# Optimization experiments

Hardware: AMD Instinct MI355X
Metric: run time of the kernel (lower is better)

The kernel has to match this reference:

```python
import jax, jax.numpy as jnp
import numpy as np
import math

B, T, C, H = 4, 4096, 1024, 16
D = C // H

def setup_inputs() -> dict:
    key = jax.random.key(0)
    k1, k2, k3, k4, k5 = jax.random.split(key, 5)
    s = 1.0 / math.sqrt(C)
    return {
        "x": jax.random.normal(k1, (B, T, C), dtype=jnp.float32),
        "W_qkv": jax.random.normal(k2, (C, 3 * C), dtype=jnp.float32) * s,
        "b_qkv": jax.random.normal(k3, (3 * C,), dtype=jnp.float32) * 0.01,
        "W_out": jax.random.normal(k4, (C, C), dtype=jnp.float32) * s,
        "b_out": jax.random.normal(k5, (C,), dtype=jnp.float32) * 0.01,
    }

def reference(x, W_qkv, b_qkv, W_out, b_out):
    qkv = x @ W_qkv + b_qkv                      # (B,T,3C)
    q, k, v = jnp.split(qkv, 3, axis=2)
    q = q.reshape(B, T, H, D)
    k = k.reshape(B, T, H, D)
    v = v.reshape(B, T, H, D)
    # attention over the HEAD axis per (B,T): scores (B,T,H,H)
    att = jnp.einsum('bthd,btgd->bthg', q, k) / math.sqrt(D)
    att = jax.nn.softmax(att, axis=-1)
    out = jnp.einsum('bthg,btgd->bthd', att, v)  # (B,T,H,D)
    out = out.reshape(B, T, C)
    return out @ W_out + b_out
```

## Files before the change

### kernel.cpp

```cpp
#include <hip/hip_runtime.h>
#include <cstdint>
#include <cstddef>

constexpr int Bc = 4;
constexpr int Tc = 4096;
constexpr int Cc = 1024;
constexpr int Hc = 16;
constexpr int Dc = 64;
constexpr int Mc = Bc * Tc;
constexpr int N1c = 3 * Cc;
constexpr int Kc = Cc;
constexpr int KBc = Kc / 32;

typedef __bf16 bf16x8 __attribute__((ext_vector_type(8)));
typedef float  f32x4  __attribute__((ext_vector_type(4)));

__device__ __forceinline__ float bf2f(unsigned short u) {
    return __uint_as_float(((unsigned)u) << 16);
}
__device__ __forceinline__ unsigned short f2bf(float f) {
    unsigned u = __float_as_uint(f);
    u += 0x7FFF + ((u >> 16) & 1);
    return (unsigned short)(u >> 16);
}


__global__ void convert_x_packed(const float* __restrict__ x,
                                 unsigned short* __restrict__ Ap) {
    const int w = threadIdx.x >> 6, lane = threadIdx.x & 63;
    const int t = blockIdx.x * 4 + w;
    const int mb = t >> 5, kb = t & 31;
    const int r = lane >> 2, c = lane & 3;
    const float* src = x + (size_t)(mb * 16 + r) * Kc + kb * 32 + c * 8;
    float4 f0 = *(const float4*)src;
    float4 f1 = *(const float4*)(src + 4);
    unsigned short u[8];
    u[0] = f2bf(f0.x); u[1] = f2bf(f0.y); u[2] = f2bf(f0.z); u[3] = f2bf(f0.w);
    u[4] = f2bf(f1.x); u[5] = f2bf(f1.y); u[6] = f2bf(f1.z); u[7] = f2bf(f1.w);
    *(uint4*)(Ap + (size_t)t * 512 + (c * 16 + r) * 8) = *(uint4*)u;
}

__global__ void transpose_convert_packed(const float* __restrict__ W,
                                         unsigned short* __restrict__ Bp,
                                         int K, int N) {
    __shared__ float tile[32][33];
    const int tx = threadIdx.x, ty = threadIdx.y;
    const int n0 = blockIdx.x * 32, k0 = blockIdx.y * 32;
    for (int i = ty; i < 32; i += 8)
        tile[i][tx] = W[(size_t)(k0 + i) * N + n0 + tx];
    __syncthreads();
    const int t = ty * 32 + tx;
    const int h = t >> 7, rr = t & 127, lane = rr >> 1, half = rr & 1;
    const int fq = lane >> 4, fn = lane & 15;
    unsigned short u[4];
    #pragma unroll
    for (int j = 0; j < 4; ++j)
        u[j] = f2bf(tile[fq * 8 + half * 4 + j][h * 16 + fn]);
    size_t tileIdx = (size_t)((n0 >> 4) + h) * (K >> 5) + (k0 >> 5);
    *(uint2*)(Bp + tileIdx * 512 + lane * 8 + half * 4) = *(uint2*)u;
}

template <bool OUT_BF16>
__global__ __launch_bounds__(256, 3) void flat_gemm_kernel(
    const unsigned short* __restrict__ Ap,
    const unsigned short* __restrict__ Bp,
    const float* __restrict__ bias,
    void* __restrict__ Cout,
    int M, int N, int K) {
    const int KB = K >> 5;
    const int w    = threadIdx.x >> 6;
    const int lane = threadIdx.x & 63;
    const int m0 = blockIdx.y * 128;
    const int n0 = blockIdx.x * 128;
    const int wm = (w >> 1) * 64;
    const int wn = (w & 1) * 64;

    const unsigned short* Abase = Ap + (size_t)(((m0 + wm) >> 4) * KB) * 512 + lane * 8;
    const unsigned short* Bbase = Bp + (size_t)(((n0 + wn) >> 4) * KB) * 512 + lane * 8;
    const int miStride = KB * 512;
    const int kbStride = 512;

    const f32x4 zero4 = {0.f, 0.f, 0.f, 0.f};
    f32x4 acc[4][4];
    #pragma unroll
    for (int i = 0; i < 4; ++i)
        #pragma unroll
        for (int j = 0; j < 4; ++j) acc[i][j] = zero4;

    bf16x8 a0[4], b0[4], a1[4], b1[4];
    #pragma unroll
    for (int mi = 0; mi < 4; ++mi) a0[mi] = *(const bf16x8*)(Abase + mi * miStride);
    #pragma unroll
    for (int ni = 0; ni < 4; ++ni) b0[ni] = *(const bf16x8*)(Bbase + ni * miStride);

    #pragma unroll 1
    for (int kb = 0; kb < KB; kb += 2) {
        #pragma unroll
        for (int mi = 0; mi < 4; ++mi)
            a1[mi] = *(const bf16x8*)(Abase + mi * miStride + (kb + 1) * kbStride);
        #pragma unroll
        for (int ni = 0; ni < 4; ++ni)
            b1[ni] = *(const bf16x8*)(Bbase + ni * miStride + (kb + 1) * kbStride);
        #pragma unroll
        for (int mi = 0; mi < 4; ++mi)
            #pragma unroll
            for (int ni = 0; ni < 4; ++ni)
                acc[mi][ni] = __builtin_amdgcn_mfma_f32_16x16x32_bf16(
                    a0[mi], b0[ni], acc[mi][ni], 0, 0, 0);
        if (kb + 2 < KB) {
            #pragma unroll
            for (int mi = 0; mi < 4; ++mi)
                a0[mi] = *(const bf16x8*)(Abase + mi * miStride + (kb + 2) * kbStride);
            #pragma unroll
            for (int ni = 0; ni < 4; ++ni)
                b0[ni] = *(const bf16x8*)(Bbase + ni * miStride + (kb + 2) * kbStride);
        }
        #pragma unroll
        for (int mi = 0; mi < 4; ++mi)
            #pragma unroll
            for (int ni = 0; ni < 4; ++ni)
                acc[mi][ni] = __builtin_amdgcn_mfma_f32_16x16x32_bf16(
                    a1[mi], b1[ni], acc[mi][ni], 0, 0, 0);
    }

    const int fr = lane & 15;
    const int fq = lane >> 4;
    #pragma unroll
    for (int mi = 0; mi < 4; ++mi) {
        #pragma unroll
        for (int ni = 0; ni < 4; ++ni) {
            int row = m0 + wm + mi * 16 + fq * 4;
            int col = n0 + wn + ni * 16 + fr;
            float bb = bias[col];
            #pragma unroll
            for (int r = 0; r < 4; ++r) {
                float v = acc[mi][ni][r] + bb;
                if (OUT_BF16)
                    ((unsigned short*)Cout)[(size_t)(row + r) * N + col] = f2bf(v);
                else
                    ((float*)Cout)[(size_t)(row + r) * N + col] = v;
            }
        }
    }
}

__global__ __launch_bounds__(256) void attn_mfma_kernel(
    const unsigned short* __restrict__ qkv,
    unsigned short* __restrict__ attP) {
    __shared__ char smem[4 * 3584];
    const int w    = threadIdx.x >> 6;
    const int lane = threadIdx.x & 63;
    const int m    = lane & 15;
    const int q    = lane >> 4;
    const int row  = blockIdx.x * 4 + w;
    unsigned short* sV = (unsigned short*)(smem + w * 3584);
    float*          sP = (float*)(smem + w * 3584 + 2304);

    const unsigned short* src = qkv + (size_t)row * 3072;

    bf16x8 aq0 = *(const bf16x8*)(src + m * 64 + q * 8);
    bf16x8 aq1 = *(const bf16x8*)(src + m * 64 + 32 + q * 8);
    bf16x8 bk0 = *(const bf16x8*)(src + 1024 + m * 64 + q * 8);
    bf16x8 bk1 = *(const bf16x8*)(src + 1024 + m * 64 + 32 + q * 8);

    #pragma unroll
    for (int t = 0; t < 2; ++t) {
        int G = t * 64 + lane;
        int r = G >> 3, p = G & 7;
        *(uint4*)(sV + r * 72 + p * 8) = *(const uint4*)(src + 2048 + G * 8);
    }

    f32x4 s = {0.f, 0.f, 0.f, 0.f};
    s = __builtin_amdgcn_mfma_f32_16x16x32_bf16(aq0, bk0, s, 0, 0, 0);
    s = __builtin_amdgcn_mfma_f32_16x16x32_bf16(aq1, bk1, s, 0, 0, 0);

    #pragma unroll
    for (int r = 0; r < 4; ++r) {
        float t0 = s[r] * 0.125f;
        float mx = t0;
        mx = fmaxf(mx, __shfl_xor(mx, 1));
        mx = fmaxf(mx, __shfl_xor(mx, 2));
        mx = fmaxf(mx, __shfl_xor(mx, 4));
        mx = fmaxf(mx, __shfl_xor(mx, 8));
        float e = __expf(t0 - mx);
        float su = e;
        su += __shfl_xor(su, 1);
        su += __shfl_xor(su, 2);
        su += __shfl_xor(su, 4);
        su += __shfl_xor(su, 8);
        sP[(q * 4 + r) * 20 + m] = e / su;
    }
    __syncthreads();

    const float* pr = sP + m * 20 + (q & 1) * 8;
    float4 pf0 = *(const float4*)(pr);
    float4 pf1 = *(const float4*)(pr + 4);
    const bool act = (q < 2);
    union { unsigned short u[8]; bf16x8 b; } pa;
    pa.u[0] = act ? f2bf(pf0.x) : 0;
    pa.u[1] = act ? f2bf(pf0.y) : 0;
    pa.u[2] = act ? f2bf(pf0.z) : 0;
    pa.u[3] = act ? f2bf(pf0.w) : 0;
    pa.u[4] = act ? f2bf(pf1.x) : 0;
    pa.u[5] = act ? f2bf(pf1.y) : 0;
    pa.u[6] = act ? f2bf(pf1.z) : 0;
    pa.u[7] = act ? f2bf(pf1.w) : 0;

    const unsigned short* vb = sV + (q & 1) * 8 * 72;
    const size_t tileBase = (size_t)(row >> 4) * 32 * 512;
    const int fr_tok = row & 15;
    #pragma unroll
    for (int c4 = 0; c4 < 4; ++c4) {
        union { unsigned short u[8]; bf16x8 b; } vf;
        #pragma unroll
        for (int j = 0; j < 8; ++j) vf.u[j] = vb[j * 72 + c4 * 16 + m];
        f32x4 o = {0.f, 0.f, 0.f, 0.f};
        o = __builtin_amdgcn_mfma_f32_16x16x32_bf16(pa.b, vf.b, o, 0, 0, 0);
        #pragma unroll
        for (int r = 0; r < 4; ++r) {
            int col = (q * 4 + r) * 64 + c4 * 16 + m;
            size_t off = tileBase + (size_t)(col >> 5) * 512
                       + (((col >> 3) & 3) * 16 + fr_tok) * 8 + (col & 7);
            attP[off] = f2bf(o[r]);
        }
    }
}

extern "C" void kernel_launch(void* const* d_in, const int* in_sizes, int n_in,
                              void* d_out, int out_size, void* d_ws, size_t ws_size,
                              hipStream_t stream) {
    const float* x    = (const float*)d_in[0];
    const float* Wqkv = (const float*)d_in[1];
    const float* bqkv = (const float*)d_in[2];
    const float* Wout = (const float*)d_in[3];
    const float* bout = (const float*)d_in[4];
    float* out = (float*)d_out;

    char* ws = (char*)d_ws;
    unsigned short* xp   = (unsigned short*)ws;                 ws += (size_t)Mc * Kc * 2;
    unsigned short* Wqkp = (unsigned short*)ws;                 ws += (size_t)N1c * Kc * 2;
    unsigned short* Wop  = (unsigned short*)ws;                 ws += (size_t)Cc * Kc * 2;
    unsigned short* qkv  = (unsigned short*)ws;
    unsigned short* attP = xp;

    convert_x_packed<<<(Mc / 16) * KBc / 4, 256, 0, stream>>>(x, xp);
    transpose_convert_packed<<<dim3(N1c / 32, Kc / 32), dim3(32, 8), 0, stream>>>(Wqkv, Wqkp, Kc, N1c);
    transpose_convert_packed<<<dim3(Cc / 32, Kc / 32), dim3(32, 8), 0, stream>>>(Wout, Wop, Kc, Cc);
    flat_gemm_kernel<true><<<dim3(N1c / 128, Mc / 128), 256, 0, stream>>>(xp, Wqkp, bqkv, qkv, Mc, N1c, Kc);
    attn_mfma_kernel<<<Mc / 4, 256, 0, stream>>>(qkv, attP);
    flat_gemm_kernel<false><<<dim3(Cc / 128, Mc / 128), 256, 0, stream>>>(attP, Wop, bout, out, Mc, Cc, Kc);
}
```

Before: 336.8 us.

## Add XCD-aware GEMM block swizzle, row-major attention output with separate repack

The GEMM grid becomes 1D and block ids are remapped so that each XCD handles a contiguous band of M tiles, grouped 8 at a time, to improve L2 reuse of the A and B tiles. The attention kernel now writes its output row-major, giving coalesced stores instead of scattered packed-tile stores. A new repack kernel then converts that output into the packed layout the GEMM expects. The GEMM occupancy hint is raised from 3 to 4 blocks per SM. The cost is an extra kernel launch and an extra 32MB round trip through memory, plus more register pressure in the GEMM.

```diff
diff --git a/kernel.cpp b/kernel.cpp
--- a/kernel.cpp
+++ b/kernel.cpp
@@ -40,6 +40,16 @@
     *(uint4*)(Ap + (size_t)t * 512 + (c * 16 + r) * 8) = *(uint4*)u;
 }
 
+__global__ void repack_bf16_packed(const unsigned short* __restrict__ src,
+                                   unsigned short* __restrict__ Ap) {
+    const int w = threadIdx.x >> 6, lane = threadIdx.x & 63;
+    const int t = blockIdx.x * 4 + w;
+    const int mb = t >> 5, kb = t & 31;
+    const int r = lane >> 2, c = lane & 3;
+    uint4 v = *(const uint4*)(src + (size_t)(mb * 16 + r) * Kc + kb * 32 + c * 8);
+    *(uint4*)(Ap + (size_t)t * 512 + (c * 16 + r) * 8) = v;
+}
+
 __global__ void transpose_convert_packed(const float* __restrict__ W,
                                          unsigned short* __restrict__ Bp,
                                          int K, int N) {
@@ -61,17 +71,27 @@
 }
 
 template <bool OUT_BF16>
-__global__ __launch_bounds__(256, 3) void flat_gemm_kernel(
+__global__ __launch_bounds__(256, 4) void flat_gemm_kernel(
     const unsigned short* __restrict__ Ap,
     const unsigned short* __restrict__ Bp,
     const float* __restrict__ bias,
     void* __restrict__ Cout,
-    int M, int N, int K) {
+    int M, int N, int K, int NB) {
     const int KB = K >> 5;
+    const int MB = M >> 7;
+    const int id   = blockIdx.x;
+    const int xcd  = id & 7;
+    const int per  = id >> 3;
+    const int MSTR = MB >> 3;
+    const int byl  = per & 7;
+    const int bx   = (per >> 3) % NB;
+    const int pass = per / (8 * NB);
+    const int by   = xcd * MSTR + pass * 8 + byl;
+
     const int w    = threadIdx.x >> 6;
     const int lane = threadIdx.x & 63;
-    const int m0 = blockIdx.y * 128;
-    const int n0 = blockIdx.x * 128;
+    const int m0 = by * 128;
+    const int n0 = bx * 128;
     const int wm = (w >> 1) * 64;
     const int wn = (w & 1) * 64;
 
@@ -146,7 +166,7 @@
 
 __global__ __launch_bounds__(256) void attn_mfma_kernel(
     const unsigned short* __restrict__ qkv,
-    unsigned short* __restrict__ attP) {
+    unsigned short* __restrict__ att) {
     __shared__ char smem[4 * 3584];
     const int w    = threadIdx.x >> 6;
     const int lane = threadIdx.x & 63;
@@ -207,8 +227,7 @@
     pa.u[7] = act ? f2bf(pf1.w) : 0;
 
     const unsigned short* vb = sV + (q & 1) * 8 * 72;
-    const size_t tileBase = (size_t)(row >> 4) * 32 * 512;
-    const int fr_tok = row & 15;
+    unsigned short* dst = att + (size_t)row * 1024;
     #pragma unroll
     for (int c4 = 0; c4 < 4; ++c4) {
         union { unsigned short u[8]; bf16x8 b; } vf;
@@ -216,13 +235,12 @@
         for (int j = 0; j < 8; ++j) vf.u[j] = vb[j * 72 + c4 * 16 + m];
         f32x4 o = {0.f, 0.f, 0.f, 0.f};
         o = __builtin_amdgcn_mfma_f32_16x16x32_bf16(pa.b, vf.b, o, 0, 0, 0);
-        #pragma unroll
-        for (int r = 0; r < 4; ++r) {
-            int col = (q * 4 + r) * 64 + c4 * 16 + m;
-            size_t off = tileBase + (size_t)(col >> 5) * 512
-                       + (((col >> 3) & 3) * 16 + fr_tok) * 8 + (col & 7);
-            attP[off] = f2bf(o[r]);
-        }
+        unsigned short outv[4];
+        #pragma unroll
+        for (int r = 0; r < 4; ++r) outv[r] = f2bf(o[r]);
+        #pragma unroll
+        for (int r = 0; r < 4; ++r)
+            dst[(q * 4 + r) * 64 + c4 * 16 + m] = outv[r];
     }
 }
 
@@ -237,16 +255,20 @@
     float* out = (float*)d_out;
 
     char* ws = (char*)d_ws;
-    unsigned short* xp   = (unsigned short*)ws;                 ws += (size_t)Mc * Kc * 2;
-    unsigned short* Wqkp = (unsigned short*)ws;                 ws += (size_t)N1c * Kc * 2;
-    unsigned short* Wop  = (unsigned short*)ws;                 ws += (size_t)Cc * Kc * 2;
-    unsigned short* qkv  = (unsigned short*)ws;
-    unsigned short* attP = xp;
+    unsigned short* xp    = (unsigned short*)ws;                ws += (size_t)Mc * Kc * 2;
+    unsigned short* Wqkp  = (unsigned short*)ws;                ws += (size_t)N1c * Kc * 2;
+    unsigned short* Wop   = (unsigned short*)ws;                ws += (size_t)Cc * Kc * 2;
+    unsigned short* qkv   = (unsigned short*)ws;                ws += (size_t)Mc * N1c * 2;
+    unsigned short* attRM = (unsigned short*)ws;
+    unsigned short* attP  = xp;
 
     convert_x_packed<<<(Mc / 16) * KBc / 4, 256, 0, stream>>>(x, xp);
     transpose_convert_packed<<<dim3(N1c / 32, Kc / 32), dim3(32, 8), 0, stream>>>(Wqkv, Wqkp, Kc, N1c);
     transpose_convert_packed<<<dim3(Cc / 32, Kc / 32), dim3(32, 8), 0, stream>>>(Wout, Wop, Kc, Cc);
-    flat_gemm_kernel<true><<<dim3(N1c / 128, Mc / 128), 256, 0, stream>>>(xp, Wqkp, bqkv, qkv, Mc, N1c, Kc);
-    attn_mfma_kernel<<<Mc / 4, 256, 0, stream>>>(qkv, attP);
-    flat_gemm_kernel<false><<<dim3(Cc / 128, Mc / 128), 256, 0, stream>>>(attP, Wop, bout, out, Mc, Cc, Kc);
-}
+    flat_gemm_kernel<true><<<(N1c / 128) * (Mc / 128), 256, 0, stream>>>(
+        xp, Wqkp, bqkv, qkv, Mc, N1c, Kc, N1c / 128);
+    attn_mfma_kernel<<<Mc / 4, 256, 0, stream>>>(qkv, attRM);
+    repack_bf16_packed<<<(Mc / 16) * KBc / 4, 256, 0, stream>>>(attRM, attP);
+    flat_gemm_kernel<false><<<(Cc / 128) * (Mc / 128), 256, 0, stream>>>(
+        attP, Wop, bout, out, Mc, Cc, Kc, Cc / 128);
+}
```

Result: no change. 332.8 us (-1.2%).

## Stage GEMM tiles through LDS with direct global-to-LDS loads and XCD-aware block mapping

Applied to the files above, without the earlier changes.

Replaces the register-only GEMM, where each wave loaded its own A/B fragments from global memory, with a version that stages 128x32 A and B tiles in shared memory via global_load_lds. Each wave now loads one quarter of the tile, so fragments are shared across the four waves instead of each fetched twice. Blocks are remapped to a 1D grid so that consecutive M-tiles land on the same XCD, improving L2 reuse. The cost is single-buffered LDS with two barriers per k-step and no prefetch overlap, which may expose load latency.

```diff
diff --git a/kernel.cpp b/kernel.cpp
--- a/kernel.cpp
+++ b/kernel.cpp
@@ -14,6 +14,8 @@
 
 typedef __bf16 bf16x8 __attribute__((ext_vector_type(8)));
 typedef float  f32x4  __attribute__((ext_vector_type(4)));
+typedef __attribute__((address_space(1))) uint32_t gu32;
+typedef __attribute__((address_space(3))) uint32_t lu32;
 
 __device__ __forceinline__ float bf2f(unsigned short u) {
     return __uint_as_float(((unsigned)u) << 16);
@@ -22,6 +24,10 @@
     unsigned u = __float_as_uint(f);
     u += 0x7FFF + ((u >> 16) & 1);
     return (unsigned short)(u >> 16);
+}
+
+__device__ __forceinline__ void load_lds16(const void* g, void* l) {
+    __builtin_amdgcn_global_load_lds((gu32*)(uintptr_t)g, (lu32*)(uintptr_t)l, 16, 0, 0);
 }
 
 
@@ -61,24 +67,43 @@
 }
 
 template <bool OUT_BF16>
-__global__ __launch_bounds__(256, 3) void flat_gemm_kernel(
+__global__ __launch_bounds__(256, 4) void lds_gemm_kernel(
     const unsigned short* __restrict__ Ap,
     const unsigned short* __restrict__ Bp,
     const float* __restrict__ bias,
     void* __restrict__ Cout,
-    int M, int N, int K) {
+    int M, int N, int K, int NB) {
+    __shared__ unsigned short sA[8 * 512];
+    __shared__ unsigned short sB[8 * 512];
     const int KB = K >> 5;
+    const int MB = M >> 7;
+    const int id   = blockIdx.x;
+    const int xcd  = id & 7;
+    const int per  = id >> 3;
+    const int MSTR = MB >> 3;
+    const int byl  = per & 7;
+    const int bx   = (per >> 3) % NB;
+    const int pass = per / (8 * NB);
+    const int by   = xcd * MSTR + pass * 8 + byl;
+
     const int w    = threadIdx.x >> 6;
     const int lane = threadIdx.x & 63;
-    const int m0 = blockIdx.y * 128;
-    const int n0 = blockIdx.x * 128;
+    const int m0 = by * 128;
+    const int n0 = bx * 128;
     const int wm = (w >> 1) * 64;
     const int wn = (w & 1) * 64;
 
-    const unsigned short* Abase = Ap + (size_t)(((m0 + wm) >> 4) * KB) * 512 + lane * 8;
-    const unsigned short* Bbase = Bp + (size_t)(((n0 + wn) >> 4) * KB) * 512 + lane * 8;
-    const int miStride = KB * 512;
-    const int kbStride = 512;
+    const unsigned short* gA0 = Ap + ((size_t)(by * 8 + w    ) * KB) * 512 + lane * 8;
+    const unsigned short* gA1 = Ap + ((size_t)(by * 8 + w + 4) * KB) * 512 + lane * 8;
+    const unsigned short* gB0 = Bp + ((size_t)(bx * 8 + w    ) * KB) * 512 + lane * 8;
+    const unsigned short* gB1 = Bp + ((size_t)(bx * 8 + w + 4) * KB) * 512 + lane * 8;
+    unsigned short* lA0 = sA + (w    ) * 512;
+    unsigned short* lA1 = sA + (w + 4) * 512;
+    unsigned short* lB0 = sB + (w    ) * 512;
+    unsigned short* lB1 = sB + (w + 4) * 512;
+
+    const unsigned short* aP = sA + (wm >> 4) * 512 + lane * 8;
+    const unsigned short* bP = sB + (wn >> 4) * 512 + lane * 8;
 
     const f32x4 zero4 = {0.f, 0.f, 0.f, 0.f};
     f32x4 acc[4][4];
@@ -87,40 +112,27 @@
         #pragma unroll
         for (int j = 0; j < 4; ++j) acc[i][j] = zero4;
 
-    bf16x8 a0[4], b0[4], a1[4], b1[4];
-    #pragma unroll
-    for (int mi = 0; mi < 4; ++mi) a0[mi] = *(const bf16x8*)(Abase + mi * miStride);
-    #pragma unroll
-    for (int ni = 0; ni < 4; ++ni) b0[ni] = *(const bf16x8*)(Bbase + ni * miStride);
-
     #pragma unroll 1
-    for (int kb = 0; kb < KB; kb += 2) {
-        #pragma unroll
-        for (int mi = 0; mi < 4; ++mi)
-            a1[mi] = *(const bf16x8*)(Abase + mi * miStride + (kb + 1) * kbStride);
-        #pragma unroll
-        for (int ni = 0; ni < 4; ++ni)
-            b1[ni] = *(const bf16x8*)(Bbase + ni * miStride + (kb + 1) * kbStride);
+    for (int kb = 0; kb < KB; ++kb) {
+        load_lds16(gA0, lA0);
+        load_lds16(gA1, lA1);
+        load_lds16(gB0, lB0);
+        load_lds16(gB1, lB1);
+        gA0 += 512; gA1 += 512; gB0 += 512; gB1 += 512;
+        __syncthreads();
+
+        bf16x8 af[4], bfr[4];
+        #pragma unroll
+        for (int mi = 0; mi < 4; ++mi) af[mi]  = *(const bf16x8*)(aP + mi * 512);
+        #pragma unroll
+        for (int ni = 0; ni < 4; ++ni) bfr[ni] = *(const bf16x8*)(bP + ni * 512);
         #pragma unroll
         for (int mi = 0; mi < 4; ++mi)
             #pragma unroll
             for (int ni = 0; ni < 4; ++ni)
                 acc[mi][ni] = __builtin_amdgcn_mfma_f32_16x16x32_bf16(
-                    a0[mi], b0[ni], acc[mi][ni], 0, 0, 0);
-        if (kb + 2 < KB) {
-            #pragma unroll
-            for (int mi = 0; mi < 4; ++mi)
-                a0[mi] = *(const bf16x8*)(Abase + mi * miStride + (kb + 2) * kbStride);
-            #pragma unroll
-            for (int ni = 0; ni < 4; ++ni)
-                b0[ni] = *(const bf16x8*)(Bbase + ni * miStride + (kb + 2) * kbStride);
-        }
-        #pragma unroll
-        for (int mi = 0; mi < 4; ++mi)
-            #pragma unroll
-            for (int ni = 0; ni < 4; ++ni)
-                acc[mi][ni] = __builtin_amdgcn_mfma_f32_16x16x32_bf16(
-                    a1[mi], b1[ni], acc[mi][ni], 0, 0, 0);
+                    af[mi], bfr[ni], acc[mi][ni], 0, 0, 0);
+        __syncthreads();
     }
 
     const int fr = lane & 15;
@@ -246,7 +258,9 @@
     convert_x_packed<<<(Mc / 16) * KBc / 4, 256, 0, stream>>>(x, xp);
     transpose_convert_packed<<<dim3(N1c / 32, Kc / 32), dim3(32, 8), 0, stream>>>(Wqkv, Wqkp, Kc, N1c);
     transpose_convert_packed<<<dim3(Cc / 32, Kc / 32), dim3(32, 8), 0, stream>>>(Wout, Wop, Kc, Cc);
-    flat_gemm_kernel<true><<<dim3(N1c / 128, Mc / 128), 256, 0, stream>>>(xp, Wqkp, bqkv, qkv, Mc, N1c, Kc);
+    lds_gemm_kernel<true><<<(N1c / 128) * (Mc / 128), 256, 0, stream>>>(
+        xp, Wqkp, bqkv, qkv, Mc, N1c, Kc, N1c / 128);
     attn_mfma_kernel<<<Mc / 4, 256, 0, stream>>>(qkv, attP);
-    flat_gemm_kernel<false><<<dim3(Cc / 128, Mc / 128), 256, 0, stream>>>(attP, Wop, bout, out, Mc, Cc, Kc);
-}
+    lds_gemm_kernel<false><<<(Cc / 128) * (Mc / 128), 256, 0, stream>>>(
+        attP, Wop, bout, out, Mc, Cc, Kc, Cc / 128);
+}
```

Measured after the change: 295.9 us. 12.2% less time.
